# Performance work log

Hardware: AMD Instinct MI355X
Metric: run time of the kernel (lower is better)

The kernel has to match this reference:

```python
import jax, jax.numpy as jnp
import numpy as np

BN_EPS = 1e-5

def setup_inputs() -> dict:
    key = jax.random.key(0)
    k1, k2, k3 = jax.random.split(key, 3)
    B, D_IN, D_OUT = 16384, 2048, 1024
    stdv = np.sqrt(1.5 / (D_IN + D_OUT))
    x = jax.random.normal(k1, (B, D_IN), dtype=jnp.float32)
    weight = jax.random.uniform(k2, (D_OUT, D_IN), dtype=jnp.float32, minval=-stdv, maxval=stdv)
    bias = jax.random.normal(k3, (D_OUT,), dtype=jnp.float32) * 0.01
    gamma = jnp.ones((D_OUT,), dtype=jnp.float32)
    beta = jnp.zeros((D_OUT,), dtype=jnp.float32)
    return {"x": x, "weight": weight, "bias": bias, "gamma": gamma, "beta": beta}

def reference(x, weight, bias, gamma, beta):
    # STE-binarized weights: forward uses sign(w) (>=0 -> +1), grad flows via clamp(w,-1,1)
    w_sign = jnp.where(weight >= 0, 1.0, -1.0).astype(weight.dtype)
    w_clip = jnp.clip(weight, -1.0, 1.0)
    w_bin = jax.lax.stop_gradient(w_sign - w_clip) + w_clip
    # y = x @ w_bin.T + bias   -> [B, D_OUT]
    y = jnp.einsum('bi,oi->bo', x, w_bin) + bias[None, :]
    # BatchNorm1d (training mode: batch statistics, biased variance)
    mean = jnp.mean(y, axis=0)
    var = jnp.mean((y - mean) ** 2, axis=0)
    y_norm = (y - mean) * jax.lax.rsqrt(var + BN_EPS)
    return y_norm * gamma + beta
```

## Files before the change

### kernel.cpp

```cpp
#include <hip/hip_runtime.h>
#include <hip/hip_bf16.h>

typedef __attribute__((ext_vector_type(4))) float f32x4;
typedef __attribute__((ext_vector_type(8))) __bf16 bf16x8;
typedef __attribute__((ext_vector_type(4))) unsigned int uint4v;

constexpr int M = 16384;
constexpr int N = 1024;
constexpr int K = 2048;
constexpr int BM = 256, BN = 256, BK = 32;
constexpr int NK = K / BK;
constexpr float BN_EPS = 1e-5f;
constexpr int TM2 = M / BM;
constexpr int GRID = (M / BM) * (N / BN);

#define GLOAD_LDS16(g, l)                                                      \
  __builtin_amdgcn_global_load_lds(                                            \
      (const __attribute__((address_space(1))) void*)(g),                      \
      (__attribute__((address_space(3))) void*)(l), 16, 0, 0)

#define SB0 __builtin_amdgcn_sched_barrier(0)

__device__ __forceinline__ unsigned sgnbf(float f) {
  return (f >= 0.f) ? 0x3F80u : 0xBF80u;
}
__global__ __launch_bounds__(256) void binw_kernel(
    const float* __restrict__ w, uint4v* __restrict__ wb,
    unsigned* __restrict__ ctr) {
  if (blockIdx.x == 0 && threadIdx.x == 0) *ctr = 0;
  size_t i = (size_t)blockIdx.x * 256 + threadIdx.x;
  const f32x4* win = (const f32x4*)w;
  f32x4 v0 = win[i * 2];
  f32x4 v1 = win[i * 2 + 1];
  uint4v o;
  o.x = sgnbf(v0[0]) | (sgnbf(v0[1]) << 16);
  o.y = sgnbf(v0[2]) | (sgnbf(v0[3]) << 16);
  o.z = sgnbf(v1[0]) | (sgnbf(v1[1]) << 16);
  o.w = sgnbf(v1[2]) | (sgnbf(v1[3]) << 16);
  wb[i] = o;
}

__global__ __launch_bounds__(1024) void gemm_bin_kernel(
    const float* __restrict__ Af, const unsigned short* __restrict__ B,
    float* __restrict__ Y, float* __restrict__ psum, float* __restrict__ psq,
    const float* __restrict__ gamma, const float* __restrict__ beta,
    unsigned* __restrict__ ctr) {
  __shared__ unsigned short As[3][BM * BK];
  __shared__ unsigned short Bs[3][BN * BK];
  __shared__ float redsum[4][BN];
  __shared__ float redsq[4][BN];

  const int tid = threadIdx.x;
  const int wid = tid >> 6;
  const int lane = tid & 63;
  const int wr = wid >> 2, wc = wid & 3;

  const int bid = blockIdx.x;
  const int swz = (bid & 7) * 32 + (bid >> 3);
  const int tm = swz >> 2, tn = swz & 3;
  const size_t m0 = (size_t)tm * BM, n0 = (size_t)tn * BN;

  const int frow = lane & 15;
  const int fcb = lane >> 4;
  const int swzc = fcb ^ ((frow >> 1) & 3);
  const int aoff = (wr * 64 + frow) * BK + swzc * 8;
  const int boff = (wc * 64 + frow) * BK + swzc * 8;

  f32x4 acc[4][4];
#pragma unroll
  for (int m = 0; m < 4; ++m)
#pragma unroll
    for (int n = 0; n < 4; ++n)
#pragma unroll
      for (int j = 0; j < 4; ++j) acc[m][n][j] = 0.f;

  const int r0s = tid >> 2;
  const int c0s = (tid & 3) ^ ((r0s >> 1) & 3);
  const unsigned short* pB = B + (n0 + r0s) * (size_t)K + c0s * 8;

  const int rA0 = tid >> 2;
  const int cA = (tid & 3) ^ ((rA0 >> 1) & 3);
  const float* pAf = Af + (m0 + rA0) * (size_t)K + cA * 8;
  const int awb0 = rA0 * 32 + (tid & 3) * 8;
  f32x4 As_[2];

#define A_ISSUE(ktv)                                                           \
  {                                                                            \
    const size_t k0_ = (size_t)(ktv)*BK;                                       \
    As_[0] = *(const f32x4*)(pAf + k0_);                                       \
    As_[1] = *(const f32x4*)(pAf + k0_ + 4);                                   \
  }
#define B_ISSUE(ss, ktv)                                                       \
  { GLOAD_LDS16(pB + (size_t)(ktv)*BK, &Bs[ss][wid * 512]); }
#define A_WRITE(ss)                                                            \
  {                                                                            \
    bf16x8 v0_;                                                                \
    _Pragma("unroll") for (int j_ = 0; j_ < 4; ++j_) {                         \
      v0_[j_] = (__bf16)As_[0][j_];                                            \
      v0_[4 + j_] = (__bf16)As_[1][j_];                                        \
    }                                                                          \
    *(bf16x8*)&As[ss][awb0] = v0_;                                             \
  }

#define WAITL                                                                  \
  asm volatile("s_waitcnt lgkmcnt(0)" ::: "memory");                           \
  __builtin_amdgcn_sched_barrier(0);

#define LDA(s, m) (*(const bf16x8*)&As[s][aoff + (m)*512])
#define LDB(s, n) (*(const bf16x8*)&Bs[s][boff + (n)*512])

#define MF(mi, av)                                                             \
  _Pragma("unroll") for (int n = 0; n < 4; ++n) acc[mi][n] =                   \
      __builtin_amdgcn_mfma_f32_16x16x32_bf16(av, b_[n], acc[mi][n], 0, 0, 0);

#define WINDOW(s, ktv, MODE)                                                   \
  {                                                                            \
    bf16x8 b_[4], a0, a1, a2, a3;                                              \
    if (MODE == 0) {                                                           \
      A_ISSUE((ktv) + 2);         \
      SB0;                                                                     \
    }                                                                          \
    b_[0] = LDB(s, 0);                                                         \
    b_[1] = LDB(s, 1);                                                         \
    b_[2] = LDB(s, 2);                                                         \
    b_[3] = LDB(s, 3);                                                         \
    a0 = LDA(s, 0);                                                            \
    a1 = LDA(s, 1);                                                            \
    if (MODE == 0) {                                                           \
      B_ISSUE(((ktv) + 2) % 3, (ktv) + 2);           \
      SB0;                                                                     \
    }                                                                          \
    WAITL                                                                      \
    __builtin_amdgcn_s_setprio(1);                                             \
    a2 = LDA(s, 2);                                                            \
    a3 = LDA(s, 3);                                                            \
    MF(0, a0)                                                                  \
    MF(1, a1)                                                                  \
    __builtin_amdgcn_s_setprio(0);                                             \
    WAITL                                                                      \
    __builtin_amdgcn_s_setprio(1);                                             \
    MF(2, a2)                                                                  \
    MF(3, a3)                                                                  \
    __builtin_amdgcn_s_setprio(0);                                             \
    SB0;                                                                       \
    if (MODE == 0) {                                                           \
      asm volatile("s_waitcnt vmcnt(1)" ::: "memory");                         \
      A_WRITE(((ktv) + 2) % 3);                                                \
    } else if (MODE == 1) {                                                    \
      asm volatile("s_waitcnt vmcnt(0)" ::: "memory");                         \
    }                                                                          \
    if (MODE != 2) {                                                           \
      asm volatile("s_waitcnt lgkmcnt(0)" ::: "memory");                       \
      __builtin_amdgcn_s_barrier();                                            \
      asm volatile("" ::: "memory");                                           \
    }                                                                          \
  }

  A_ISSUE(0);
  SB0;
  B_ISSUE(0, 0);
  SB0;
  asm volatile("s_waitcnt vmcnt(1)" ::: "memory");
  A_WRITE(0);
  A_ISSUE(1);
  SB0;
  B_ISSUE(1, 1);
  SB0;
  asm volatile("s_waitcnt vmcnt(1)" ::: "memory");
  A_WRITE(1);
  asm volatile("s_waitcnt lgkmcnt(0)" ::: "memory");
  __builtin_amdgcn_s_barrier();
  asm volatile("" ::: "memory");

  for (int kt = 0; kt < NK - 4; kt += 3) {
    WINDOW(0, kt, 0);
    WINDOW(1, kt + 1, 0);
    WINDOW(2, kt + 2, 0);
  }
  WINDOW(0, NK - 4, 0);
  WINDOW(1, NK - 3, 0);
  WINDOW(2, NK - 2, 1);
  WINDOW(0, NK - 1, 2);

  float cs[4], cq[4];
#pragma unroll
  for (int n = 0; n < 4; ++n) {
    float s = 0.f, q = 0.f;
#pragma unroll
    for (int m = 0; m < 4; ++m)
#pragma unroll
      for (int j = 0; j < 4; ++j) {
        float v = acc[m][n][j];
        s += v;
        q += v * v;
      }
    cs[n] = s;
    cq[n] = q;
  }
#pragma unroll
  for (int n = 0; n < 4; ++n) {
    cs[n] += __shfl_xor(cs[n], 16);
    cs[n] += __shfl_xor(cs[n], 32);
    cq[n] += __shfl_xor(cq[n], 16);
    cq[n] += __shfl_xor(cq[n], 32);
  }
  __syncthreads();
  if (fcb == 0) {
#pragma unroll
    for (int n = 0; n < 4; ++n) {
      redsum[wr][wc * 64 + n * 16 + frow] = cs[n];
      redsq[wr][wc * 64 + n * 16 + frow] = cq[n];
    }
  }
  __syncthreads();
  if (tid < BN) {
    const size_t c = n0 + tid;
    psum[(size_t)tm * N + c] =
        redsum[0][tid] + redsum[1][tid] + redsum[2][tid] + redsum[3][tid];
    psq[(size_t)tm * N + c] =
        redsq[0][tid] + redsq[1][tid] + redsq[2][tid] + redsq[3][tid];
  }

  __syncthreads();
  if (tid == 0) {
    __threadfence();
    const unsigned ticket = __hip_atomic_fetch_add(
        ctr, 1u, __ATOMIC_RELAXED, __HIP_MEMORY_SCOPE_AGENT);
    const unsigned goal = (ticket & ~255u) + 256u;
    while ((int)(__hip_atomic_load(ctr, __ATOMIC_RELAXED,
                                   __HIP_MEMORY_SCOPE_AGENT) -
                 goal) < 0) {
      __builtin_amdgcn_s_sleep(16);
    }
    __threadfence();
  }
  __syncthreads();

  const int cl = tid & 255;
  const int qd = tid >> 8;
  {
    float s = 0.f, q = 0.f;
    const float* ps = psum + n0 + cl;
    const float* pq = psq + n0 + cl;
    for (int i = qd * 16; i < qd * 16 + 16; ++i) {
      s += ps[(size_t)i * N];
      q += pq[(size_t)i * N];
    }
    redsum[qd][cl] = s;
    redsq[qd][cl] = q;
  }
  __syncthreads();
  if (tid < 256) {
    const float S =
        redsum[0][cl] + redsum[1][cl] + redsum[2][cl] + redsum[3][cl];
    const float Q = redsq[0][cl] + redsq[1][cl] + redsq[2][cl] + redsq[3][cl];
    const float mean = S * (1.f / (float)M);
    const float var = Q * (1.f / (float)M) - mean * mean;
    const float inv = rsqrtf(var + BN_EPS);
    const float sc = gamma[n0 + cl] * inv;
    redsum[0][cl] = sc;
    redsq[0][cl] = beta[n0 + cl] - mean * sc;
  }
  __syncthreads();

#pragma unroll
  for (int m = 0; m < 4; ++m) {
    const size_t r0 = m0 + wr * 64 + m * 16 + fcb * 4;
#pragma unroll
    for (int n = 0; n < 4; ++n) {
      const int cloc = wc * 64 + n * 16 + frow;
      const float sc = redsum[0][cloc];
      const float sh = redsq[0][cloc];
      float* yp = Y + r0 * N + n0 + cloc;
#pragma unroll
      for (int j = 0; j < 4; ++j) yp[(size_t)j * N] = acc[m][n][j] * sc + sh;
    }
  }
}

extern "C" void kernel_launch(void* const* d_in, const int* in_sizes, int n_in,
                              void* d_out, int out_size, void* d_ws,
                              size_t ws_size, hipStream_t stream) {
  const float* x = (const float*)d_in[0];
  const float* w = (const float*)d_in[1];
  const float* gamma = (const float*)d_in[3];
  const float* beta = (const float*)d_in[4];
  float* Y = (float*)d_out;

  char* ws = (char*)d_ws;
  uint4v* wb = (uint4v*)ws;
  float* psum = (float*)(ws + (size_t)N * K * 2);
  float* psq = psum + (size_t)TM2 * N;
  unsigned* ctr = (unsigned*)(psq + (size_t)TM2 * N);

  binw_kernel<<<(N * K / 8) / 256, 256, 0, stream>>>(w, wb, ctr);

  const unsigned short* Bp = (const unsigned short*)wb;
  void* args[] = {(void*)&x,   (void*)&Bp,    (void*)&Y,    (void*)&psum,
                  (void*)&psq, (void*)&gamma, (void*)&beta, (void*)&ctr};
  hipLaunchCooperativeKernel(reinterpret_cast<void*>(gemm_bin_kernel),
                             dim3(GRID), dim3(1024), args, 0, stream);
}
```

Before: 119.5 us.

## Restructure GEMM to 512 threads, BK=64 double-buffer, per-column last-block BN stats

```diff
diff --git a/kernel.cpp b/kernel.cpp
--- a/kernel.cpp
+++ b/kernel.cpp
@@ -8,8 +8,8 @@
 constexpr int M = 16384;
 constexpr int N = 1024;
 constexpr int K = 2048;
-constexpr int BM = 256, BN = 256, BK = 32;
-constexpr int NK = K / BK;
+constexpr int BM = 256, BN = 256, BK = 64;
+constexpr int NK2 = K / BK;
 constexpr float BN_EPS = 1e-5f;
 constexpr int TM2 = M / BM;
 constexpr int GRID = (M / BM) * (N / BN);
@@ -20,6 +20,9 @@
       (__attribute__((address_space(3))) void*)(l), 16, 0, 0)
 
 #define SB0 __builtin_amdgcn_sched_barrier(0)
+#define BARRIER __builtin_amdgcn_s_barrier()
+#define VMC(n) asm volatile("s_waitcnt vmcnt(" #n ")" ::: "memory")
+#define LGKM0 asm volatile("s_waitcnt lgkmcnt(0)" ::: "memory")
 
 __device__ __forceinline__ unsigned sgnbf(float f) {
   return (f >= 0.f) ? 0x3F80u : 0xBF80u;
@@ -27,7 +30,7 @@
 __global__ __launch_bounds__(256) void binw_kernel(
     const float* __restrict__ w, uint4v* __restrict__ wb,
     unsigned* __restrict__ ctr) {
-  if (blockIdx.x == 0 && threadIdx.x == 0) *ctr = 0;
+  if (blockIdx.x == 0 && threadIdx.x < 8) ctr[threadIdx.x] = 0;
   size_t i = (size_t)blockIdx.x * 256 + threadIdx.x;
   const f32x4* win = (const f32x4*)w;
   f32x4 v0 = win[i * 2];
@@ -40,15 +43,17 @@
   wb[i] = o;
 }
 
-__global__ __launch_bounds__(1024) void gemm_bin_kernel(
+__global__ __launch_bounds__(512) void gemm_bin_kernel(
     const float* __restrict__ Af, const unsigned short* __restrict__ B,
     float* __restrict__ Y, float* __restrict__ psum, float* __restrict__ psq,
+    float* __restrict__ scale, float* __restrict__ shift,
     const float* __restrict__ gamma, const float* __restrict__ beta,
     unsigned* __restrict__ ctr) {
-  __shared__ unsigned short As[3][BM * BK];
-  __shared__ unsigned short Bs[3][BN * BK];
-  __shared__ float redsum[4][BN];
-  __shared__ float redsq[4][BN];
+  __shared__ unsigned short As[2][BM * BK];
+  __shared__ unsigned short Bs[2][BN * BK];
+  __shared__ float redsum[2][BN];
+  __shared__ float redsq[2][BN];
+  __shared__ unsigned sh_tkt;
 
   const int tid = threadIdx.x;
   const int wid = tid >> 6;
@@ -62,218 +67,263 @@
 
   const int frow = lane & 15;
   const int fcb = lane >> 4;
-  const int swzc = fcb ^ ((frow >> 1) & 3);
-  const int aoff = (wr * 64 + frow) * BK + swzc * 8;
-  const int boff = (wc * 64 + frow) * BK + swzc * 8;
-
-  f32x4 acc[4][4];
-#pragma unroll
-  for (int m = 0; m < 4; ++m)
-#pragma unroll
-    for (int n = 0; n < 4; ++n)
-#pragma unroll
-      for (int j = 0; j < 4; ++j) acc[m][n][j] = 0.f;
-
-  const int r0s = tid >> 2;
-  const int c0s = (tid & 3) ^ ((r0s >> 1) & 3);
-  const unsigned short* pB = B + (n0 + r0s) * (size_t)K + c0s * 8;
-
-  const int rA0 = tid >> 2;
-  const int cA = (tid & 3) ^ ((rA0 >> 1) & 3);
-  const float* pAf = Af + (m0 + rA0) * (size_t)K + cA * 8;
-  const int awb0 = rA0 * 32 + (tid & 3) * 8;
-  f32x4 As_[2];
-
-#define A_ISSUE(ktv)                                                           \
+  const int f7 = frow & 7;
+  const int aoff0 = (wr * 128 + frow) * 64 + (fcb ^ f7) * 8;
+  const int aoff1 = (wr * 128 + frow) * 64 + ((4 + fcb) ^ f7) * 8;
+  const int boff0 = (wc * 64 + frow) * 64 + (fcb ^ f7) * 8;
+  const int boff1 = (wc * 64 + frow) * 64 + ((4 + fcb) ^ f7) * 8;
+
+  f32x4 acc[8][4];
+#pragma unroll
+  for (int mi = 0; mi < 8; ++mi)
+#pragma unroll
+    for (int nj = 0; nj < 4; ++nj)
+#pragma unroll
+      for (int j = 0; j < 4; ++j) acc[mi][nj][j] = 0.f;
+
+  const int rbase = wid * 8 + (lane >> 3);
+  const int cg = (lane & 7) ^ ((lane >> 3) & 7);
+  const unsigned short* pBg = B + (n0 + rbase) * (size_t)K + cg * 8;
+
+  const int rA = tid >> 1;
+  const int hA = tid & 1;
+  const int hA8 = hA * 8;
+  const float* pA = Af + (m0 + rA) * (size_t)K;
+  const int awb0 = rA * 64 + ((0 + hA) ^ (rA & 7)) * 8;
+  const int awb1 = rA * 64 + ((2 + hA) ^ (rA & 7)) * 8;
+  const int awb2 = rA * 64 + ((4 + hA) ^ (rA & 7)) * 8;
+  const int awb3 = rA * 64 + ((6 + hA) ^ (rA & 7)) * 8;
+
+#define AL(g, ktv, R0, R1)                                                     \
   {                                                                            \
-    const size_t k0_ = (size_t)(ktv)*BK;                                       \
-    As_[0] = *(const f32x4*)(pAf + k0_);                                       \
-    As_[1] = *(const f32x4*)(pAf + k0_ + 4);                                   \
-  }
-#define B_ISSUE(ss, ktv)                                                       \
-  { GLOAD_LDS16(pB + (size_t)(ktv)*BK, &Bs[ss][wid * 512]); }
-#define A_WRITE(ss)                                                            \
+    const float* p_ = pA + (size_t)(ktv)*64 + (g)*16 + hA8;                    \
+    R0 = *(const f32x4*)p_;                                                    \
+    R1 = *(const f32x4*)(p_ + 4);                                              \
+  }
+#define AW(g, NS, R0, R1)                                                      \
   {                                                                            \
-    bf16x8 v0_;                                                                \
+    bf16x8 v_;                                                                 \
     _Pragma("unroll") for (int j_ = 0; j_ < 4; ++j_) {                         \
-      v0_[j_] = (__bf16)As_[0][j_];                                            \
-      v0_[4 + j_] = (__bf16)As_[1][j_];                                        \
-    }                                                                          \
-    *(bf16x8*)&As[ss][awb0] = v0_;                                             \
-  }
-
-#define WAITL                                                                  \
-  asm volatile("s_waitcnt lgkmcnt(0)" ::: "memory");                           \
-  __builtin_amdgcn_sched_barrier(0);
-
-#define LDA(s, m) (*(const bf16x8*)&As[s][aoff + (m)*512])
-#define LDB(s, n) (*(const bf16x8*)&Bs[s][boff + (n)*512])
-
-#define MF(mi, av)                                                             \
-  _Pragma("unroll") for (int n = 0; n < 4; ++n) acc[mi][n] =                   \
-      __builtin_amdgcn_mfma_f32_16x16x32_bf16(av, b_[n], acc[mi][n], 0, 0, 0);
-
-#define WINDOW(s, ktv, MODE)                                                   \
+      v_[j_] = (__bf16)R0[j_];                                                 \
+      v_[4 + j_] = (__bf16)R1[j_];                                             \
+    }                                                                          \
+    *(bf16x8*)&As[NS][awb##g] = v_;                                            \
+  }
+#define BG(rd, ktv, NS)                                                        \
+  GLOAD_LDS16(pBg + (size_t)(rd)*64 * K + (size_t)(ktv)*64,                    \
+              &Bs[NS][((rd)*64 + wid * 8) * 64])
+
+#define LDA(S, KS, mi)                                                         \
+  (*(const bf16x8*)&As[S][((KS) ? aoff1 : aoff0) + (mi)*1024])
+#define LDB(S, KS, nj)                                                         \
+  (*(const bf16x8*)&Bs[S][((KS) ? boff1 : boff0) + (nj)*1024])
+
+#define PH_READ_B(S, KS)                                                       \
+  b_[0] = LDB(S, KS, 0);                                                       \
+  b_[1] = LDB(S, KS, 1);                                                       \
+  b_[2] = LDB(S, KS, 2);                                                       \
+  b_[3] = LDB(S, KS, 3);
+#define PH_READ_A(S, KS, MB)                                                   \
+  a_[0] = LDA(S, KS, MB + 0);                                                  \
+  a_[1] = LDA(S, KS, MB + 1);                                                  \
+  a_[2] = LDA(S, KS, MB + 2);                                                  \
+  a_[3] = LDA(S, KS, MB + 3);
+
+#define PH_MFMA(MB)                                                            \
+  LGKM0;                                                                       \
+  SB0;                                                                         \
+  __builtin_amdgcn_s_setprio(1);                                               \
+  _Pragma("unroll") for (int d_ = 0; d_ < 4; ++d_)                             \
+      _Pragma("unroll") for (int nj_ = 0; nj_ < 4; ++nj_) acc[(MB) + d_][nj_] =\
+          __builtin_amdgcn_mfma_f32_16x16x32_bf16(a_[d_], b_[nj_],             \
+                                                  acc[(MB) + d_][nj_], 0, 0,   \
+                                                  0);                          \
+  __builtin_amdgcn_s_setprio(0);
+
+#define ITER(S, NS, ktn, STG)                                                  \
   {                                                                            \
-    bf16x8 b_[4], a0, a1, a2, a3;                                              \
-    if (MODE == 0) {                                                           \
-      A_ISSUE((ktv) + 2);         \
-      SB0;                                                                     \
-    }                                                                          \
-    b_[0] = LDB(s, 0);                                                         \
-    b_[1] = LDB(s, 1);                                                         \
-    b_[2] = LDB(s, 2);                                                         \
-    b_[3] = LDB(s, 3);                                                         \
-    a0 = LDA(s, 0);                                                            \
-    a1 = LDA(s, 1);                                                            \
-    if (MODE == 0) {                                                           \
-      B_ISSUE(((ktv) + 2) % 3, (ktv) + 2);           \
-      SB0;                                                                     \
-    }                                                                          \
-    WAITL                                                                      \
-    __builtin_amdgcn_s_setprio(1);                                             \
-    a2 = LDA(s, 2);                                                            \
-    a3 = LDA(s, 3);                                                            \
-    MF(0, a0)                                                                  \
-    MF(1, a1)                                                                  \
-    __builtin_amdgcn_s_setprio(0);                                             \
-    WAITL                                                                      \
-    __builtin_amdgcn_s_setprio(1);                                             \
-    MF(2, a2)                                                                  \
-    MF(3, a3)                                                                  \
-    __builtin_amdgcn_s_setprio(0);                                             \
+    bf16x8 b_[4], a_[4];                                                       \
+                    \
+    PH_READ_B(S, 0);                                                           \
+    PH_READ_A(S, 0, 0);                                                        \
     SB0;                                                                       \
-    if (MODE == 0) {                                                           \
-      asm volatile("s_waitcnt vmcnt(1)" ::: "memory");                         \
-      A_WRITE(((ktv) + 2) % 3);                                                \
-    } else if (MODE == 1) {                                                    \
-      asm volatile("s_waitcnt vmcnt(0)" ::: "memory");                         \
-    }                                                                          \
-    if (MODE != 2) {                                                           \
-      asm volatile("s_waitcnt lgkmcnt(0)" ::: "memory");                       \
-      __builtin_amdgcn_s_barrier();                                            \
-      asm volatile("" ::: "memory");                                           \
-    }                                                                          \
-  }
-
-  A_ISSUE(0);
-  SB0;
-  B_ISSUE(0, 0);
-  SB0;
-  asm volatile("s_waitcnt vmcnt(1)" ::: "memory");
-  A_WRITE(0);
-  A_ISSUE(1);
-  SB0;
-  B_ISSUE(1, 1);
-  SB0;
-  asm volatile("s_waitcnt vmcnt(1)" ::: "memory");
-  A_WRITE(1);
-  asm volatile("s_waitcnt lgkmcnt(0)" ::: "memory");
-  __builtin_amdgcn_s_barrier();
-  asm volatile("" ::: "memory");
-
-  for (int kt = 0; kt < NK - 4; kt += 3) {
-    WINDOW(0, kt, 0);
-    WINDOW(1, kt + 1, 0);
-    WINDOW(2, kt + 2, 0);
-  }
-  WINDOW(0, NK - 4, 0);
-  WINDOW(1, NK - 3, 0);
-  WINDOW(2, NK - 2, 1);
-  WINDOW(0, NK - 1, 2);
-
-  float cs[4], cq[4];
-#pragma unroll
-  for (int n = 0; n < 4; ++n) {
+    if (STG) {                                                                 \
+      AL(0, ktn, s00, s01);                                                    \
+      AL(1, ktn, s10, s11);                                                    \
+      SB0;                                                                     \
+      BG(0, ktn, NS);                                                          \
+      BG(1, ktn, NS);                                                          \
+      SB0;                                                                     \
+    }                                                                          \
+    BARRIER;                                                                   \
+    PH_MFMA(0);                                                                \
+    BARRIER;                                                                   \
+          \
+    PH_READ_A(S, 0, 4);                                                        \
+    SB0;                                                                       \
+    if (STG) {                                                                 \
+      VMC(2);                                                                  \
+      AW(0, NS, s00, s01);                                                     \
+      AW(1, NS, s10, s11);                                                     \
+      SB0;                                                                     \
+      AL(2, ktn, s00, s01);                                                    \
+      AL(3, ktn, s10, s11);                                                    \
+      SB0;                                                                     \
+      BG(2, ktn, NS);                                                          \
+      BG(3, ktn, NS);                                                          \
+      SB0;                                                                     \
+    }                                                                          \
+    BARRIER;                                                                   \
+    PH_MFMA(4);                                                                \
+    BARRIER;                                                                   \
+                        \
+    PH_READ_B(S, 1);                                                           \
+    PH_READ_A(S, 1, 0);                                                        \
+    SB0;                                                                       \
+    if (STG) {                                                                 \
+      VMC(2);                                                                  \
+      AW(2, NS, s00, s01);                                                     \
+      AW(3, NS, s10, s11);                                                     \
+      SB0;                                                                     \
+    }                                                                          \
+    BARRIER;                                                                   \
+    PH_MFMA(0);                                                                \
+    BARRIER;                                                                   \
+                \
+    PH_READ_A(S, 1, 4);                                                        \
+    SB0;                                                                       \
+    if (STG) {                                                                 \
+      VMC(0);                                                                  \
+    }                                                                          \
+    BARRIER;                                                                   \
+    PH_MFMA(4);                                                                \
+    LGKM0;                                                                     \
+    BARRIER;                                                                   \
+  }
+
+  f32x4 s00, s01, s10, s11;
+  {
+    f32x4 s20, s21, s30, s31;
+    AL(0, 0, s00, s01);
+    AL(1, 0, s10, s11);
+    SB0;
+    AL(2, 0, s20, s21);
+    AL(3, 0, s30, s31);
+    SB0;
+    BG(0, 0, 0);
+    BG(1, 0, 0);
+    BG(2, 0, 0);
+    BG(3, 0, 0);
+    SB0;
+    VMC(4);
+    AW(0, 0, s00, s01);
+    AW(1, 0, s10, s11);
+    AW(2, 0, s20, s21);
+    AW(3, 0, s30, s31);
+    VMC(0);
+    LGKM0;
+    BARRIER;
+  }
+
+  for (int kt = 0; kt < NK2 - 2; kt += 2) {
+    ITER(0, 1, kt + 1, 1);
+    ITER(1, 0, kt + 2, 1);
+  }
+  ITER(0, 1, NK2 - 1, 1);
+  ITER(1, 0, 0, 0);
+
+#pragma unroll
+  for (int nj = 0; nj < 4; ++nj) {
     float s = 0.f, q = 0.f;
 #pragma unroll
-    for (int m = 0; m < 4; ++m)
+    for (int mi = 0; mi < 8; ++mi)
 #pragma unroll
       for (int j = 0; j < 4; ++j) {
-        float v = acc[m][n][j];
+        float v = acc[mi][nj][j];
         s += v;
         q += v * v;
       }
-    cs[n] = s;
-    cq[n] = q;
-  }
-#pragma unroll
-  for (int n = 0; n < 4; ++n) {
-    cs[n] += __shfl_xor(cs[n], 16);
-    cs[n] += __shfl_xor(cs[n], 32);
-    cq[n] += __shfl_xor(cq[n], 16);
-    cq[n] += __shfl_xor(cq[n], 32);
-  }
-  __syncthreads();
-  if (fcb == 0) {
-#pragma unroll
-    for (int n = 0; n < 4; ++n) {
-      redsum[wr][wc * 64 + n * 16 + frow] = cs[n];
-      redsq[wr][wc * 64 + n * 16 + frow] = cq[n];
+    s += __shfl_xor(s, 16);
+    s += __shfl_xor(s, 32);
+    q += __shfl_xor(q, 16);
+    q += __shfl_xor(q, 32);
+    if (fcb == 0) {
+      redsum[wr][wc * 64 + nj * 16 + frow] = s;
+      redsq[wr][wc * 64 + nj * 16 + frow] = q;
     }
   }
   __syncthreads();
   if (tid < BN) {
-    const size_t c = n0 + tid;
-    psum[(size_t)tm * N + c] =
-        redsum[0][tid] + redsum[1][tid] + redsum[2][tid] + redsum[3][tid];
-    psq[(size_t)tm * N + c] =
-        redsq[0][tid] + redsq[1][tid] + redsq[2][tid] + redsq[3][tid];
-  }
-
-  __syncthreads();
+    psum[(size_t)tm * N + n0 + tid] = redsum[0][tid] + redsum[1][tid];
+    psq[(size_t)tm * N + n0 + tid] = redsq[0][tid] + redsq[1][tid];
+  }
+  __syncthreads();
+
   if (tid == 0) {
     __threadfence();
-    const unsigned ticket = __hip_atomic_fetch_add(
-        ctr, 1u, __ATOMIC_RELAXED, __HIP_MEMORY_SCOPE_AGENT);
-    const unsigned goal = (ticket & ~255u) + 256u;
-    while ((int)(__hip_atomic_load(ctr, __ATOMIC_RELAXED,
-                                   __HIP_MEMORY_SCOPE_AGENT) -
-                 goal) < 0) {
-      __builtin_amdgcn_s_sleep(16);
-    }
-    __threadfence();
-  }
-  __syncthreads();
-
-  const int cl = tid & 255;
-  const int qd = tid >> 8;
-  {
-    float s = 0.f, q = 0.f;
-    const float* ps = psum + n0 + cl;
-    const float* pq = psq + n0 + cl;
-    for (int i = qd * 16; i < qd * 16 + 16; ++i) {
-      s += ps[(size_t)i * N];
-      q += pq[(size_t)i * N];
-    }
-    redsum[qd][cl] = s;
-    redsq[qd][cl] = q;
-  }
-  __syncthreads();
-  if (tid < 256) {
-    const float S =
-        redsum[0][cl] + redsum[1][cl] + redsum[2][cl] + redsum[3][cl];
-    const float Q = redsq[0][cl] + redsq[1][cl] + redsq[2][cl] + redsq[3][cl];
-    const float mean = S * (1.f / (float)M);
-    const float var = Q * (1.f / (float)M) - mean * mean;
-    const float inv = rsqrtf(var + BN_EPS);
-    const float sc = gamma[n0 + cl] * inv;
-    redsum[0][cl] = sc;
-    redsq[0][cl] = beta[n0 + cl] - mean * sc;
-  }
-  __syncthreads();
-
-#pragma unroll
-  for (int m = 0; m < 4; ++m) {
-    const size_t r0 = m0 + wr * 64 + m * 16 + fcb * 4;
-#pragma unroll
-    for (int n = 0; n < 4; ++n) {
-      const int cloc = wc * 64 + n * 16 + frow;
+    sh_tkt = __hip_atomic_fetch_add(&ctr[tn], 1u, __ATOMIC_RELAXED,
+                                    __HIP_MEMORY_SCOPE_AGENT);
+  }
+  __syncthreads();
+  if (sh_tkt == TM2 - 1) {
+    if (tid == 0) __threadfence();
+    __syncthreads();
+    {
+      const int c = tid & 255, h = tid >> 8;
+      float s = 0.f, q = 0.f;
+      const float* ps = psum + n0 + c;
+      const float* pq = psq + n0 + c;
+      for (int i = h * 32; i < h * 32 + 32; ++i) {
+        s += ps[(size_t)i * N];
+        q += pq[(size_t)i * N];
+      }
+      redsum[h][c] = s;
+      redsq[h][c] = q;
+    }
+    __syncthreads();
+    if (tid < BN) {
+      const float S = redsum[0][tid] + redsum[1][tid];
+      const float Q = redsq[0][tid] + redsq[1][tid];
+      const float mean = S * (1.f / (float)M);
+      const float var = Q * (1.f / (float)M) - mean * mean;
+      const float inv = rsqrtf(var + BN_EPS);
+      const float sc = gamma[n0 + tid] * inv;
+      scale[n0 + tid] = sc;
+      shift[n0 + tid] = beta[n0 + tid] - mean * sc;
+    }
+    __syncthreads();
+    if (tid == 0) {
+      __threadfence();
+      __hip_atomic_store(&ctr[4 + tn], 1u, __ATOMIC_RELAXED,
+                         __HIP_MEMORY_SCOPE_AGENT);
+    }
+  } else {
+    if (tid == 0) {
+      while (__hip_atomic_load(&ctr[4 + tn], __ATOMIC_RELAXED,
+                               __HIP_MEMORY_SCOPE_AGENT) == 0u) {
+        __builtin_amdgcn_s_sleep(8);
+      }
+      __threadfence();
+    }
+  }
+  __syncthreads();
+
+  if (tid < BN) {
+    redsum[0][tid] = scale[n0 + tid];
+    redsq[0][tid] = shift[n0 + tid];
+  }
+  __syncthreads();
+#pragma unroll
+  for (int mi = 0; mi < 8; ++mi) {
+    const size_t r0 = m0 + wr * 128 + mi * 16 + fcb * 4;
+#pragma unroll
+    for (int nj = 0; nj < 4; ++nj) {
+      const int cloc = wc * 64 + nj * 16 + frow;
       const float sc = redsum[0][cloc];
       const float sh = redsq[0][cloc];
       float* yp = Y + r0 * N + n0 + cloc;
 #pragma unroll
-      for (int j = 0; j < 4; ++j) yp[(size_t)j * N] = acc[m][n][j] * sc + sh;
+      for (int j = 0; j < 4; ++j) yp[(size_t)j * N] = acc[mi][nj][j] * sc + sh;
     }
   }
 }
@@ -291,13 +341,18 @@
   uint4v* wb = (uint4v*)ws;
   float* psum = (float*)(ws + (size_t)N * K * 2);
   float* psq = psum + (size_t)TM2 * N;
-  unsigned* ctr = (unsigned*)(psq + (size_t)TM2 * N);
+  float* scale = psq + (size_t)TM2 * N;
+  float* shift = scale + N;
+  unsigned* ctr = (unsigned*)(shift + N);
 
   binw_kernel<<<(N * K / 8) / 256, 256, 0, stream>>>(w, wb, ctr);
 
+  const float* xp = x;
   const unsigned short* Bp = (const unsigned short*)wb;
-  void* args[] = {(void*)&x,   (void*)&Bp,    (void*)&Y,    (void*)&psum,
-                  (void*)&psq, (void*)&gamma, (void*)&beta, (void*)&ctr};
+  void* args[] = {(void*)&xp,    (void*)&Bp,    (void*)&Y,
+                  (void*)&psum,  (void*)&psq,   (void*)&scale,
+                  (void*)&shift, (void*)&gamma, (void*)&beta,
+                  (void*)&ctr};
   hipLaunchCooperativeKernel(reinterpret_cast<void*>(gemm_bin_kernel),
-                             dim3(GRID), dim3(1024), args, 0, stream);
+                             dim3(GRID), dim3(512), args, 0, stream);
 }
```

Result: slower. 128.3 us (+7.4%).
